# Kernel optimization log

Hardware: AMD Instinct MI355X
Metric: run time of the kernel (lower is better)

## Reference

```python
import jax, jax.numpy as jnp
import numpy as np

N, D_IN, D_OUT, E = 8192, 2048, 2048, 8


def setup_inputs() -> dict:
    key = jax.random.key(0)
    k0, k1, k2, k3, k4, k5 = jax.random.split(key, 6)
    s = 1.0 / np.sqrt(D_IN)  # torch nn.Linear default init range
    return {
        "inputs": jax.random.normal(k0, (N, D_IN), jnp.float32),
        "condition": jax.random.normal(k1, (N, D_IN), jnp.float32),
        "Wp": jax.random.uniform(k2, (E, D_IN), jnp.float32, -s, s),
        "bp": jax.random.uniform(k3, (E,), jnp.float32, -s, s),
        "We": jax.random.uniform(k4, (E, D_OUT, D_IN), jnp.float32, -s, s),
        "be": jax.random.uniform(k5, (E, D_OUT), jnp.float32, -s, s),
    }


def reference(inputs, condition, Wp, bp, We, be):
    # predictor: gating logits [N, E]
    prediction = condition @ Wp.T + bp
    # straight-through multiplier: value == 1, gradient flows to prediction
    multiply = jnp.ones_like(prediction) + (prediction - jax.lax.stop_gradient(prediction))
    # run ALL experts on the full batch (faithful to the original): [E, N, F]
    expert_out = jnp.einsum('nd,efd->enf', inputs, We) + be[:, None, :]
    combined = multiply.T[:, :, None] * expert_out  # [E, N, F]
    # select the argmax expert per row
    idx = jnp.argmax(prediction, axis=-1)  # [N]
    result = combined[idx, jnp.arange(prediction.shape[0])]  # [N, F]
    return result
```

## Files before the change

kernel.cpp:

```cpp
#include <hip/hip_runtime.h>
#include <hip/hip_bf16.h>
#include <stdint.h>

#define N_ROWS 8192
#define DIN 2048
#define DOUT 2048
#define NE 8

#define BM3 320
#define BN3 256
#define BK2 64
#define RT3 33
#define NBLK3 (8 * RT3)

#define BM 128
#define BN 128
#define BK 64
#define MAX_RT 71

typedef __bf16 bf16x8 __attribute__((ext_vector_type(8)));
typedef float f32x4 __attribute__((ext_vector_type(4)));

__device__ __forceinline__ uint32_t f2bf(float f) {
  uint32_t u = __builtin_bit_cast(uint32_t, f);
  uint32_t r = u + 0x7FFFu + ((u >> 16) & 1u);
  return r >> 16;
}

__device__ __forceinline__ void gl2lds16(const void* g, void* l) {
  __builtin_amdgcn_global_load_lds(
      (const __attribute__((address_space(1))) unsigned int*)g,
      (__attribute__((address_space(3))) unsigned int*)l, 16, 0, 0);
}

__global__ __launch_bounds__(256) void gate_kernel(
    const float* __restrict__ cond, const float* __restrict__ Wp,
    const float* __restrict__ bp, int* __restrict__ idx, int* __restrict__ counts)
{
  __shared__ int lc[NE];
  const int t = threadIdx.x;
  if (t < NE) lc[t] = 0;

  const int lane = t & 63;
  const int wid  = t >> 6;
  const int row  = blockIdx.x * 4 + wid;

  double acc[NE];
  #pragma unroll
  for (int e = 0; e < NE; ++e) acc[e] = 0.0;

  const float4* crow = (const float4*)(cond + (size_t)row * DIN);
  const float4* wp4  = (const float4*)Wp;
  #pragma unroll
  for (int i = 0; i < DIN / 256; ++i) {
    float4 c = crow[i * 64 + lane];
    #pragma unroll
    for (int e = 0; e < NE; ++e) {
      float4 w = wp4[e * (DIN / 4) + i * 64 + lane];
      acc[e] += (double)c.x * w.x + (double)c.y * w.y
              + (double)c.z * w.z + (double)c.w * w.w;
    }
  }
  #pragma unroll
  for (int e = 0; e < NE; ++e) {
    double v = acc[e];
    #pragma unroll
    for (int off = 32; off > 0; off >>= 1) v += __shfl_down(v, off, 64);
    acc[e] = v;
  }
  __syncthreads();
  if (lane == 0) {
    int best = 0; double bv = acc[0] + (double)bp[0];
    #pragma unroll
    for (int e = 1; e < NE; ++e) {
      double v = acc[e] + (double)bp[e];
      if (v > bv) { bv = v; best = e; }
    }
    idx[row] = best;
    atomicAdd(&lc[best], 1);
  }
  __syncthreads();
  if (t < NE && lc[t] > 0) atomicAdd(&counts[t], lc[t]);
}

__global__ void scan_kernel(const int* __restrict__ counts, int* __restrict__ offsets) {
  if (threadIdx.x == 0 && blockIdx.x == 0) {
    int s = 0;
    for (int e = 0; e < NE; ++e) { offsets[e] = s; s += counts[e]; }
  }
}

__global__ __launch_bounds__(256) void scatter_kernel(
    const int* __restrict__ idx, const int* __restrict__ offsets,
    int* __restrict__ fill, int* __restrict__ rows)
{
  __shared__ int lc[NE], lb[NE];
  const int t = threadIdx.x;
  if (t < NE) lc[t] = 0;
  __syncthreads();
  int n = blockIdx.x * 256 + t;
  int e = idx[n];
  int my = atomicAdd(&lc[e], 1);
  __syncthreads();
  if (t < NE) lb[t] = (lc[t] > 0) ? atomicAdd(&fill[t], lc[t]) : 0;
  __syncthreads();
  rows[offsets[e] + lb[e] + my] = n;
}

__global__ __launch_bounds__(256) void conv_kernel(
    const float* __restrict__ src, __hip_bfloat16* __restrict__ dst, size_t nchunks)
{
  const size_t stride = (size_t)gridDim.x * 256;
  for (size_t c = (size_t)blockIdx.x * 256 + threadIdx.x; c < nchunks; c += stride) {
    float4 v0 = ((const float4*)src)[c * 2];
    float4 v1 = ((const float4*)src)[c * 2 + 1];
    uint4 o;
    o.x = f2bf(v0.x) | (f2bf(v0.y) << 16);
    o.y = f2bf(v0.z) | (f2bf(v0.w) << 16);
    o.z = f2bf(v1.x) | (f2bf(v1.y) << 16);
    o.w = f2bf(v1.z) | (f2bf(v1.w) << 16);
    ((uint4*)dst)[c] = o;
  }
}

__global__ __launch_bounds__(512, 1) void moe_gemm8(
    const __hip_bfloat16* __restrict__ Xb, const __hip_bfloat16* __restrict__ Web,
    const float* __restrict__ be, const int* __restrict__ counts,
    const int* __restrict__ rows, float* __restrict__ out)
{
  __shared__ __align__(16) __hip_bfloat16 Asm[2][2][160 * 64];
  __shared__ __align__(16) __hip_bfloat16 Bsm[2][2][128 * 64];
  __shared__ int rowid[BM3];

  const int bid = blockIdx.x;
  const int w = (bid & 7) * RT3 + (bid >> 3);
  const int ct = w / RT3;
  const int rt = w % RT3;

  int e = 0, racc = 0, cnt = 0, base = 0;
  for (; e < NE; ++e) {
    cnt = counts[e];
    int tiles = (cnt + BM3 - 1) / BM3;
    if (rt < racc + tiles) break;
    racc += tiles; base += cnt;
  }
  if (e == NE) return;
  const int row0 = (rt - racc) * BM3;
  const int tid = threadIdx.x;
  if (tid < BM3)
    rowid[tid] = (row0 + tid < cnt) ? rows[base + row0 + tid] : -1;
  __syncthreads();

  const int lane = tid & 63, wid = tid >> 6;
  const bool w4 = (wid < 4);
  const int wm = wid >> 2, wn = wid & 3;
  const int g = lane >> 4, fr = lane & 15;
  const int rsw = fr * 64 + ((g ^ ((fr >> 1) & 3)) << 4);

  const int cA0 = w4 ? (3 * wid) : (12 + 2 * (wid - 4));
  const int cA1 = cA0 + 1;
  const int cA2 = cA0 + 2;
  const int cB0 = 2 * wid, cB1 = cB0 + 1;

  const int aD0 = cA0 * 1024 + lane * 16;
  const int aD1 = cA1 * 1024 + lane * 16;
  const int aD2 = cA2 * 1024 + lane * 16;
  const int bD0 = cB0 * 1024 + lane * 16;
  const int bD1 = cB1 * 1024 + lane * 16;

  const int frs = lane >> 2;
  const int qx  = (lane & 3) ^ ((lane >> 3) & 3);
  const __hip_bfloat16 *aP[2][3], *bP[2][2];
  {
    const int cA[3] = {cA0, cA1, cA2};
    const int cB[2] = {cB0, cB1};
    #pragma unroll
    for (int h = 0; h < 2; ++h) {
      #pragma unroll
      for (int s = 0; s < 3; ++s) {
        int c = cA[s];
        int R = h * 160 + (c >> 1) * 16 + frs;
        int gr = rowid[R];
        if (gr < 0) gr = 0;
        aP[h][s] = Xb + (size_t)gr * DIN + (c & 1) * 32 + qx * 8;
      }
      #pragma unroll
      for (int s = 0; s < 2; ++s) {
        int c = cB[s];
        size_t wrow = (size_t)e * DOUT + ct * BN3 + h * 128 + (c >> 1) * 16 + frs;
        bP[h][s] = Web + wrow * DIN + (c & 1) * 32 + qx * 8;
      }
    }
  }

  f32x4 acc[2][2][5][2];
  #pragma unroll
  for (int a = 0; a < 2; ++a)
    #pragma unroll
    for (int b = 0; b < 2; ++b)
      #pragma unroll
      for (int m = 0; m < 5; ++m)
        #pragma unroll
        for (int n = 0; n < 2; ++n)
          acc[a][b][m][n] = 0.0f;

  bf16x8 av[2][5], bv[2][2];

#define STG_A(buf, h, kel) do {                                              \
    gl2lds16(aP[h][0] + (kel), (char*)&Asm[buf][h][0] + aD0);                \
    gl2lds16(aP[h][1] + (kel), (char*)&Asm[buf][h][0] + aD1);                \
    if (w4) gl2lds16(aP[h][2] + (kel), (char*)&Asm[buf][h][0] + aD2);        \
  } while (0)
#define STG_B(buf, h, kel) do {                                              \
    gl2lds16(bP[h][0] + (kel), (char*)&Bsm[buf][h][0] + bD0);                \
    gl2lds16(bP[h][1] + (kel), (char*)&Bsm[buf][h][0] + bD1); } while (0)

#define READ_A(c, h) do { const char* Ab_ = (const char*)&Asm[c][h][0];      \
    _Pragma("unroll") for (int kk = 0; kk < 2; ++kk)                         \
    _Pragma("unroll") for (int mi = 0; mi < 5; ++mi)                         \
      av[kk][mi] = *(const bf16x8*)(Ab_ + (wm * 5 + mi) * 2048 + kk * 1024 + rsw); } while (0)

#define READ_B(c, h) do { const char* Bb_ = (const char*)&Bsm[c][h][0];      \
    _Pragma("unroll") for (int kk = 0; kk < 2; ++kk)                         \
    _Pragma("unroll") for (int ni = 0; ni < 2; ++ni)                         \
      bv[kk][ni] = *(const bf16x8*)(Bb_ + (wn * 2 + ni) * 2048 + kk * 1024 + rsw); } while (0)

#define BAR   __builtin_amdgcn_s_barrier()
#define LGKM0 do { asm volatile("s_waitcnt lgkmcnt(0)" ::: "memory");        \
                   __builtin_amdgcn_sched_barrier(0); } while (0)
#define VMCN  do { if (w4) { asm volatile("s_waitcnt vmcnt(5)" ::: "memory"); } \
                   else    { asm volatile("s_waitcnt vmcnt(4)" ::: "memory"); } \
                   __builtin_amdgcn_sched_barrier(0); } while (0)
#define VMC0  do { asm volatile("s_waitcnt vmcnt(0)" ::: "memory");          \
                   __builtin_amdgcn_sched_barrier(0); } while (0)

#define MFMA_PH(mh, nh) do { __builtin_amdgcn_s_setprio(1);                  \
    _Pragma("unroll") for (int kk = 0; kk < 2; ++kk)                         \
    _Pragma("unroll") for (int mi = 0; mi < 5; ++mi)                         \
    _Pragma("unroll") for (int ni = 0; ni < 2; ++ni)                         \
      acc[mh][nh][mi][ni] = __builtin_amdgcn_mfma_f32_16x16x32_bf16(         \
          av[kk][mi], bv[kk][ni], acc[mh][nh][mi][ni], 0, 0, 0);             \
    __builtin_amdgcn_s_setprio(0); } while (0)

  STG_A(0, 0, 0);  STG_B(0, 0, 0);  STG_A(0, 1, 0);  STG_B(0, 1, 0);
  STG_A(1, 0, 64); STG_B(1, 0, 64);
  VMCN;
  BAR;

  const int T = DIN / BK2;
  #pragma unroll 1
  for (int t = 0; t < T; ++t) {
    const int c = t & 1, o = c ^ 1;
    const int k1 = (t + 1) * BK2, k2 = (t + 2) * BK2;
    const bool s1 = (t + 1 < T), s2 = (t + 2 < T);

    READ_A(c, 0); READ_B(c, 0);
    if (s1) STG_A(o, 1, k1);
    BAR; LGKM0;
    MFMA_PH(0, 0);
    BAR;

    READ_B(c, 1);
    if (s1) STG_B(o, 1, k1);
    BAR; LGKM0;
    MFMA_PH(0, 1);
    BAR;

    READ_A(c, 1); READ_B(c, 0);
    if (s2) STG_A(c, 0, k2);
    BAR; LGKM0;
    MFMA_PH(1, 0);
    BAR;

    READ_B(c, 1);
    if (s2) STG_B(c, 0, k2);
    BAR; LGKM0;
    MFMA_PH(1, 1);
    if (s2) { VMCN; } else { VMC0; }
    BAR;
  }

#undef STG_A
#undef STG_B
#undef READ_A
#undef READ_B
#undef MFMA_PH

  float beh[2][2];
  #pragma unroll
  for (int nh = 0; nh < 2; ++nh)
    #pragma unroll
    for (int ni = 0; ni < 2; ++ni)
      beh[nh][ni] = be[(size_t)e * DOUT + ct * BN3 + nh * 128 + wn * 32 + ni * 16 + fr];

  #pragma unroll
  for (int mh = 0; mh < 2; ++mh)
    #pragma unroll
    for (int mi = 0; mi < 5; ++mi)
      #pragma unroll
      for (int j = 0; j < 4; ++j) {
        int R = mh * 160 + wm * 80 + mi * 16 + g * 4 + j;
        int grow = rowid[R];
        if (grow < 0) continue;
        float* orow = out + (size_t)grow * DOUT + ct * BN3;
        #pragma unroll
        for (int nh = 0; nh < 2; ++nh)
          #pragma unroll
          for (int ni = 0; ni < 2; ++ni)
            orow[nh * 128 + wn * 32 + ni * 16 + fr] = acc[mh][nh][mi][ni][j] + beh[nh][ni];
      }
}

__global__ __launch_bounds__(256) void moe_gemm_fb(
    const float* __restrict__ X, const float* __restrict__ We,
    const float* __restrict__ be, const int* __restrict__ counts,
    const int* __restrict__ offsets, const int* __restrict__ rows,
    float* __restrict__ out)
{
  __shared__ __align__(16) unsigned char Asb[BM * BK * 2];
  __shared__ __align__(16) unsigned char Bsb[BN * BK * 2];
  __shared__ int rowid[BM];

  const int ct = blockIdx.x;
  const int rt = blockIdx.y;

  int e = 0, racc = 0, cnt = 0;
  for (; e < NE; ++e) {
    cnt = counts[e];
    int tiles = (cnt + BM - 1) / BM;
    if (rt < racc + tiles) break;
    racc += tiles;
  }
  if (e == NE) return;
  const int row0 = (rt - racc) * BM;
  const int base = offsets[e];

  if (threadIdx.x < BM) {
    int r = row0 + threadIdx.x;
    rowid[threadIdx.x] = (r < cnt) ? rows[base + r] : -1;
  }
  __syncthreads();

  const int t    = threadIdx.x;
  const int lane = t & 63;
  const int wv   = t >> 6;
  const int wr   = wv >> 1, wc = wv & 1;
  const int g    = lane >> 4, fr = lane & 15;
  const int srow = t >> 4;
  const int skq  = t & 15;

  f32x4 acc[4][4];
  #pragma unroll
  for (int m = 0; m < 4; ++m)
    #pragma unroll
    for (int n = 0; n < 4; ++n)
      acc[m][n] = 0.0f;

  const size_t bcol0 = (size_t)e * DOUT + (size_t)ct * BN;

  for (int k0 = 0; k0 < DIN; k0 += BK) {
    #pragma unroll
    for (int p = 0; p < 8; ++p) {
      int r = p * 16 + srow;
      int gr = rowid[r];
      float4 v = make_float4(0.f, 0.f, 0.f, 0.f);
      if (gr >= 0)
        v = *(const float4*)(X + (size_t)gr * DIN + k0 + skq * 4);
      uint32_t w0 = f2bf(v.x) | (f2bf(v.y) << 16);
      uint32_t w1 = f2bf(v.z) | (f2bf(v.w) << 16);
      int byte = r * (BK * 2) + ((skq * 8) ^ ((r & 7) << 4));
      *(uint2*)(Asb + byte) = make_uint2(w0, w1);
    }
    #pragma unroll
    for (int p = 0; p < 8; ++p) {
      int r = p * 16 + srow;
      float4 v = *(const float4*)(We + (bcol0 + r) * DIN + k0 + skq * 4);
      uint32_t w0 = f2bf(v.x) | (f2bf(v.y) << 16);
      uint32_t w1 = f2bf(v.z) | (f2bf(v.w) << 16);
      int byte = r * (BK * 2) + ((skq * 8) ^ ((r & 7) << 4));
      *(uint2*)(Bsb + byte) = make_uint2(w0, w1);
    }
    __syncthreads();

    #pragma unroll
    for (int kk = 0; kk < BK; kk += 32) {
      bf16x8 av[4], bv[4];
      #pragma unroll
      for (int m = 0; m < 4; ++m) {
        int r = wr * 64 + m * 16 + fr;
        int byte = r * (BK * 2) + ((((kk + g * 8) * 2)) ^ ((r & 7) << 4));
        av[m] = *(const bf16x8*)(Asb + byte);
      }
      #pragma unroll
      for (int n = 0; n < 4; ++n) {
        int c = wc * 64 + n * 16 + fr;
        int byte = c * (BK * 2) + ((((kk + g * 8) * 2)) ^ ((c & 7) << 4));
        bv[n] = *(const bf16x8*)(Bsb + byte);
      }
      #pragma unroll
      for (int m = 0; m < 4; ++m)
        #pragma unroll
        for (int n = 0; n < 4; ++n)
          acc[m][n] = __builtin_amdgcn_mfma_f32_16x16x32_bf16(av[m], bv[n], acc[m][n], 0, 0, 0);
    }
    __syncthreads();
  }

  const float* berow = be + (size_t)e * DOUT + (size_t)ct * BN + wc * 64;
  #pragma unroll
  for (int m = 0; m < 4; ++m) {
    #pragma unroll
    for (int j = 0; j < 4; ++j) {
      int r = wr * 64 + m * 16 + g * 4 + j;
      int grow = rowid[r];
      if (grow < 0) continue;
      float* orow = out + (size_t)grow * DOUT + (size_t)ct * BN + wc * 64;
      #pragma unroll
      for (int n = 0; n < 4; ++n)
        orow[n * 16 + fr] = acc[m][n][j] + berow[n * 16 + fr];
    }
  }
}

extern "C" void kernel_launch(void* const* d_in, const int* in_sizes, int n_in,
                              void* d_out, int out_size, void* d_ws, size_t ws_size,
                              hipStream_t stream) {
  const float* X    = (const float*)d_in[0];
  const float* cond = (const float*)d_in[1];
  const float* Wp   = (const float*)d_in[2];
  const float* bp   = (const float*)d_in[3];
  const float* We   = (const float*)d_in[4];
  const float* be   = (const float*)d_in[5];
  float* out = (float*)d_out;

  int* counts  = (int*)d_ws;
  int* offsets = counts + 8;
  int* fill    = counts + 16;
  int* idx     = (int*)((char*)d_ws + 256);
  int* rows    = idx + N_ROWS;
  const size_t XB_OFF  = 65792;
  const size_t WEB_OFF = XB_OFF + (size_t)N_ROWS * DIN * 2;
  const size_t WS_NEED = WEB_OFF + (size_t)NE * DOUT * DIN * 2;

  hipMemsetAsync(d_ws, 0, 256, stream);
  gate_kernel<<<N_ROWS / 4, 256, 0, stream>>>(cond, Wp, bp, idx, counts);
  scan_kernel<<<1, 64, 0, stream>>>(counts, offsets);
  scatter_kernel<<<N_ROWS / 256, 256, 0, stream>>>(idx, offsets, fill, rows);

  if (ws_size >= WS_NEED) {
    __hip_bfloat16* Xb  = (__hip_bfloat16*)((char*)d_ws + XB_OFF);
    __hip_bfloat16* Web = (__hip_bfloat16*)((char*)d_ws + WEB_OFF);
    conv_kernel<<<2048, 256, 0, stream>>>(X, Xb, (size_t)N_ROWS * DIN / 8);
    conv_kernel<<<2048, 256, 0, stream>>>(We, Web, (size_t)NE * DOUT * DIN / 8);
    moe_gemm8<<<NBLK3, 512, 0, stream>>>(Xb, Web, be, counts, rows, out);
  } else {
    moe_gemm_fb<<<dim3(DOUT / BN, MAX_RT), 256, 0, stream>>>(X, We, be, counts, offsets, rows, out);
  }
}
```

Before: 197.2 us.

## Fuse expert weight bf16 conversion into GEMM B-tile staging

Drops the separate pass that converted the full fp32 expert weight tensor to bf16. The GEMM now loads fp32 weight tiles into registers, converts them, and writes them to LDS, with restructured vmcnt waits to keep the prefetch pipeline. This removes a full read-write pass over the weights and shrinks workspace, at the cost of more global bytes per B tile, register-staged loads instead of direct-to-LDS, and extra conversion ALU work inside the main loop.

```diff
diff --git a/kernel.cpp b/kernel.cpp
--- a/kernel.cpp
+++ b/kernel.cpp
@@ -124,7 +124,7 @@
 }
 
 __global__ __launch_bounds__(512, 1) void moe_gemm8(
-    const __hip_bfloat16* __restrict__ Xb, const __hip_bfloat16* __restrict__ Web,
+    const __hip_bfloat16* __restrict__ Xb, const float* __restrict__ We,
     const float* __restrict__ be, const int* __restrict__ counts,
     const int* __restrict__ rows, float* __restrict__ out)
 {
@@ -170,7 +170,8 @@
 
   const int frs = lane >> 2;
   const int qx  = (lane & 3) ^ ((lane >> 3) & 3);
-  const __hip_bfloat16 *aP[2][3], *bP[2][2];
+  const __hip_bfloat16 *aP[2][3];
+  const float *bPf[2][2];
   {
     const int cA[3] = {cA0, cA1, cA2};
     const int cB[2] = {cB0, cB1};
@@ -188,7 +189,7 @@
       for (int s = 0; s < 2; ++s) {
         int c = cB[s];
         size_t wrow = (size_t)e * DOUT + ct * BN3 + h * 128 + (c >> 1) * 16 + frs;
-        bP[h][s] = Web + wrow * DIN + (c & 1) * 32 + qx * 8;
+        bPf[h][s] = We + wrow * DIN + (c & 1) * 32 + qx * 8;
       }
     }
   }
@@ -205,15 +206,32 @@
           acc[a][b][m][n] = 0.0f;
 
   bf16x8 av[2][5], bv[2][2];
+  float4 br1[4], br2[4];
 
 #define STG_A(buf, h, kel) do {                                              \
     gl2lds16(aP[h][0] + (kel), (char*)&Asm[buf][h][0] + aD0);                \
     gl2lds16(aP[h][1] + (kel), (char*)&Asm[buf][h][0] + aD1);                \
     if (w4) gl2lds16(aP[h][2] + (kel), (char*)&Asm[buf][h][0] + aD2);        \
   } while (0)
-#define STG_B(buf, h, kel) do {                                              \
-    gl2lds16(bP[h][0] + (kel), (char*)&Bsm[buf][h][0] + bD0);                \
-    gl2lds16(bP[h][1] + (kel), (char*)&Bsm[buf][h][0] + bD1); } while (0)
+
+#define BL(dst, h, kel) do {                                                 \
+    dst[0] = *(const float4*)(bPf[h][0] + (kel));                            \
+    dst[1] = *(const float4*)(bPf[h][0] + (kel) + 4);                        \
+    dst[2] = *(const float4*)(bPf[h][1] + (kel));                            \
+    dst[3] = *(const float4*)(bPf[h][1] + (kel) + 4); } while (0)
+
+#define BW(src, buf, h) do {                                                 \
+    uint4 o0, o1;                                                            \
+    o0.x = f2bf(src[0].x) | (f2bf(src[0].y) << 16);                          \
+    o0.y = f2bf(src[0].z) | (f2bf(src[0].w) << 16);                          \
+    o0.z = f2bf(src[1].x) | (f2bf(src[1].y) << 16);                          \
+    o0.w = f2bf(src[1].z) | (f2bf(src[1].w) << 16);                          \
+    o1.x = f2bf(src[2].x) | (f2bf(src[2].y) << 16);                          \
+    o1.y = f2bf(src[2].z) | (f2bf(src[2].w) << 16);                          \
+    o1.z = f2bf(src[3].x) | (f2bf(src[3].y) << 16);                          \
+    o1.w = f2bf(src[3].z) | (f2bf(src[3].w) << 16);                          \
+    *(uint4*)((char*)&Bsm[buf][h][0] + bD0) = o0;                            \
+    *(uint4*)((char*)&Bsm[buf][h][0] + bD1) = o1; } while (0)
 
 #define READ_A(c, h) do { const char* Ab_ = (const char*)&Asm[c][h][0];      \
     _Pragma("unroll") for (int kk = 0; kk < 2; ++kk)                         \
@@ -226,13 +244,19 @@
       bv[kk][ni] = *(const bf16x8*)(Bb_ + (wn * 2 + ni) * 2048 + kk * 1024 + rsw); } while (0)
 
 #define BAR   __builtin_amdgcn_s_barrier()
-#define LGKM0 do { asm volatile("s_waitcnt lgkmcnt(0)" ::: "memory");        \
-                   __builtin_amdgcn_sched_barrier(0); } while (0)
-#define VMCN  do { if (w4) { asm volatile("s_waitcnt vmcnt(5)" ::: "memory"); } \
-                   else    { asm volatile("s_waitcnt vmcnt(4)" ::: "memory"); } \
-                   __builtin_amdgcn_sched_barrier(0); } while (0)
-#define VMC0  do { asm volatile("s_waitcnt vmcnt(0)" ::: "memory");          \
-                   __builtin_amdgcn_sched_barrier(0); } while (0)
+#define SB0   __builtin_amdgcn_sched_barrier(0)
+#define LGKM0 do { asm volatile("s_waitcnt lgkmcnt(0)" ::: "memory"); SB0; } while (0)
+#define VMC0  do { asm volatile("s_waitcnt vmcnt(0)" ::: "memory"); SB0; } while (0)
+#define VMW1_S do { if (w4) { asm volatile("s_waitcnt vmcnt(7)" ::: "memory"); }  \
+                    else    { asm volatile("s_waitcnt vmcnt(6)" ::: "memory"); }  \
+                    SB0; } while (0)
+#define VMW1_L do { asm volatile("s_waitcnt vmcnt(2)" ::: "memory"); SB0; } while (0)
+#define VMW2   do { if (w4) { asm volatile("s_waitcnt vmcnt(6)" ::: "memory"); }  \
+                    else    { asm volatile("s_waitcnt vmcnt(4)" ::: "memory"); }  \
+                    SB0; } while (0)
+#define VMCN   do { if (w4) { asm volatile("s_waitcnt vmcnt(3)" ::: "memory"); }  \
+                    else    { asm volatile("s_waitcnt vmcnt(2)" ::: "memory"); }  \
+                    SB0; } while (0)
 
 #define MFMA_PH(mh, nh) do { __builtin_amdgcn_s_setprio(1);                  \
     _Pragma("unroll") for (int kk = 0; kk < 2; ++kk)                         \
@@ -242,9 +266,12 @@
           av[kk][mi], bv[kk][ni], acc[mh][nh][mi][ni], 0, 0, 0);             \
     __builtin_amdgcn_s_setprio(0); } while (0)
 
-  STG_A(0, 0, 0);  STG_B(0, 0, 0);  STG_A(0, 1, 0);  STG_B(0, 1, 0);
-  STG_A(1, 0, 64); STG_B(1, 0, 64);
+  BL(br1, 0, 0);  VMC0; BW(br1, 0, 0);
+  BL(br1, 1, 0);  VMC0; BW(br1, 0, 1);
+  BL(br1, 0, 64); VMC0; BW(br1, 1, 0);
+  STG_A(0, 0, 0); STG_A(0, 1, 0); STG_A(1, 0, 64);
   VMCN;
+  asm volatile("s_waitcnt lgkmcnt(0)" ::: "memory");
   BAR;
 
   const int T = DIN / BK2;
@@ -255,13 +282,17 @@
     const bool s1 = (t + 1 < T), s2 = (t + 2 < T);
 
     READ_A(c, 0); READ_B(c, 0);
+    if (s1) BL(br1, 1, k1);
+    SB0;
+    if (s2) BL(br2, 0, k2);
+    SB0;
     if (s1) STG_A(o, 1, k1);
     BAR; LGKM0;
     MFMA_PH(0, 0);
     BAR;
 
     READ_B(c, 1);
-    if (s1) STG_B(o, 1, k1);
+    if (s1) { if (s2) { VMW1_S; } else { VMW1_L; } BW(br1, o, 1); }
     BAR; LGKM0;
     MFMA_PH(0, 1);
     BAR;
@@ -273,7 +304,7 @@
     BAR;
 
     READ_B(c, 1);
-    if (s2) STG_B(c, 0, k2);
+    if (s2) { VMW2; BW(br2, c, 0); }
     BAR; LGKM0;
     MFMA_PH(1, 1);
     if (s2) { VMCN; } else { VMC0; }
@@ -281,7 +312,8 @@
   }
 
 #undef STG_A
-#undef STG_B
+#undef BL
+#undef BW
 #undef READ_A
 #undef READ_B
 #undef MFMA_PH
@@ -439,8 +471,7 @@
   int* idx     = (int*)((char*)d_ws + 256);
   int* rows    = idx + N_ROWS;
   const size_t XB_OFF  = 65792;
-  const size_t WEB_OFF = XB_OFF + (size_t)N_ROWS * DIN * 2;
-  const size_t WS_NEED = WEB_OFF + (size_t)NE * DOUT * DIN * 2;
+  const size_t WS_NEED = XB_OFF + (size_t)N_ROWS * DIN * 2;
 
   hipMemsetAsync(d_ws, 0, 256, stream);
   gate_kernel<<<N_ROWS / 4, 256, 0, stream>>>(cond, Wp, bp, idx, counts);
@@ -448,11 +479,9 @@
   scatter_kernel<<<N_ROWS / 256, 256, 0, stream>>>(idx, offsets, fill, rows);
 
   if (ws_size >= WS_NEED) {
-    __hip_bfloat16* Xb  = (__hip_bfloat16*)((char*)d_ws + XB_OFF);
-    __hip_bfloat16* Web = (__hip_bfloat16*)((char*)d_ws + WEB_OFF);
+    __hip_bfloat16* Xb = (__hip_bfloat16*)((char*)d_ws + XB_OFF);
     conv_kernel<<<2048, 256, 0, stream>>>(X, Xb, (size_t)N_ROWS * DIN / 8);
-    conv_kernel<<<2048, 256, 0, stream>>>(We, Web, (size_t)NE * DOUT * DIN / 8);
-    moe_gemm8<<<NBLK3, 512, 0, stream>>>(Xb, Web, be, counts, rows, out);
+    moe_gemm8<<<NBLK3, 512, 0, stream>>>(Xb, We, be, counts, rows, out);
   } else {
     moe_gemm_fb<<<dim3(DOUT / BN, MAX_RT), 256, 0, stream>>>(X, We, be, counts, offsets, rows, out);
   }
```

Measured after the change: 506.8 us. 2.57x slower.

## Make grouped GEMM persistent with a CU-sized grid looping over live tiles

Applied to the files above, without the earlier changes.

Launches a fixed grid of 256 blocks that loop over the actual number of row/column tiles computed from expert counts, instead of a fixed 264-block grid with early exits. Tile ordering changes so column tiles are the fastest index, grouping blocks that share the same gathered input rows. This aims to avoid a partial second wave and idle blocks, at the cost of extra barriers and per-tile setup inside the loop and different L2 reuse of weights.

```diff
diff --git a/kernel.cpp b/kernel.cpp
--- a/kernel.cpp
+++ b/kernel.cpp
@@ -10,8 +10,7 @@
 #define BM3 320
 #define BN3 256
 #define BK2 64
-#define RT3 33
-#define NBLK3 (8 * RT3)
+#define GRID3 256
 
 #define BM 128
 #define BN 128
@@ -132,25 +131,7 @@
   __shared__ __align__(16) __hip_bfloat16 Bsm[2][2][128 * 64];
   __shared__ int rowid[BM3];
 
-  const int bid = blockIdx.x;
-  const int w = (bid & 7) * RT3 + (bid >> 3);
-  const int ct = w / RT3;
-  const int rt = w % RT3;
-
-  int e = 0, racc = 0, cnt = 0, base = 0;
-  for (; e < NE; ++e) {
-    cnt = counts[e];
-    int tiles = (cnt + BM3 - 1) / BM3;
-    if (rt < racc + tiles) break;
-    racc += tiles; base += cnt;
-  }
-  if (e == NE) return;
-  const int row0 = (rt - racc) * BM3;
   const int tid = threadIdx.x;
-  if (tid < BM3)
-    rowid[tid] = (row0 + tid < cnt) ? rows[base + row0 + tid] : -1;
-  __syncthreads();
-
   const int lane = tid & 63, wid = tid >> 6;
   const bool w4 = (wid < 4);
   const int wm = wid >> 2, wn = wid & 3;
@@ -161,50 +142,26 @@
   const int cA1 = cA0 + 1;
   const int cA2 = cA0 + 2;
   const int cB0 = 2 * wid, cB1 = cB0 + 1;
-
   const int aD0 = cA0 * 1024 + lane * 16;
   const int aD1 = cA1 * 1024 + lane * 16;
   const int aD2 = cA2 * 1024 + lane * 16;
   const int bD0 = cB0 * 1024 + lane * 16;
   const int bD1 = cB1 * 1024 + lane * 16;
-
   const int frs = lane >> 2;
   const int qx  = (lane & 3) ^ ((lane >> 3) & 3);
-  const __hip_bfloat16 *aP[2][3], *bP[2][2];
-  {
-    const int cA[3] = {cA0, cA1, cA2};
-    const int cB[2] = {cB0, cB1};
-    #pragma unroll
-    for (int h = 0; h < 2; ++h) {
-      #pragma unroll
-      for (int s = 0; s < 3; ++s) {
-        int c = cA[s];
-        int R = h * 160 + (c >> 1) * 16 + frs;
-        int gr = rowid[R];
-        if (gr < 0) gr = 0;
-        aP[h][s] = Xb + (size_t)gr * DIN + (c & 1) * 32 + qx * 8;
-      }
-      #pragma unroll
-      for (int s = 0; s < 2; ++s) {
-        int c = cB[s];
-        size_t wrow = (size_t)e * DOUT + ct * BN3 + h * 128 + (c >> 1) * 16 + frs;
-        bP[h][s] = Web + wrow * DIN + (c & 1) * 32 + qx * 8;
-      }
-    }
-  }
-
-  f32x4 acc[2][2][5][2];
-  #pragma unroll
-  for (int a = 0; a < 2; ++a)
-    #pragma unroll
-    for (int b = 0; b < 2; ++b)
-      #pragma unroll
-      for (int m = 0; m < 5; ++m)
-        #pragma unroll
-        for (int n = 0; n < 2; ++n)
-          acc[a][b][m][n] = 0.0f;
-
-  bf16x8 av[2][5], bv[2][2];
+
+  int RT = 0;
+  #pragma unroll
+  for (int e = 0; e < NE; ++e) RT += (counts[e] + BM3 - 1) / BM3;
+  const int total = RT * 8;
+
+#define BAR   __builtin_amdgcn_s_barrier()
+#define SB0   __builtin_amdgcn_sched_barrier(0)
+#define LGKM0 do { asm volatile("s_waitcnt lgkmcnt(0)" ::: "memory"); SB0; } while (0)
+#define VMCN  do { if (w4) { asm volatile("s_waitcnt vmcnt(5)" ::: "memory"); } \
+                   else    { asm volatile("s_waitcnt vmcnt(4)" ::: "memory"); } \
+                   SB0; } while (0)
+#define VMC0  do { asm volatile("s_waitcnt vmcnt(0)" ::: "memory"); SB0; } while (0)
 
 #define STG_A(buf, h, kel) do {                                              \
     gl2lds16(aP[h][0] + (kel), (char*)&Asm[buf][h][0] + aD0);                \
@@ -225,15 +182,6 @@
     _Pragma("unroll") for (int ni = 0; ni < 2; ++ni)                         \
       bv[kk][ni] = *(const bf16x8*)(Bb_ + (wn * 2 + ni) * 2048 + kk * 1024 + rsw); } while (0)
 
-#define BAR   __builtin_amdgcn_s_barrier()
-#define LGKM0 do { asm volatile("s_waitcnt lgkmcnt(0)" ::: "memory");        \
-                   __builtin_amdgcn_sched_barrier(0); } while (0)
-#define VMCN  do { if (w4) { asm volatile("s_waitcnt vmcnt(5)" ::: "memory"); } \
-                   else    { asm volatile("s_waitcnt vmcnt(4)" ::: "memory"); } \
-                   __builtin_amdgcn_sched_barrier(0); } while (0)
-#define VMC0  do { asm volatile("s_waitcnt vmcnt(0)" ::: "memory");          \
-                   __builtin_amdgcn_sched_barrier(0); } while (0)
-
 #define MFMA_PH(mh, nh) do { __builtin_amdgcn_s_setprio(1);                  \
     _Pragma("unroll") for (int kk = 0; kk < 2; ++kk)                         \
     _Pragma("unroll") for (int mi = 0; mi < 5; ++mi)                         \
@@ -242,42 +190,122 @@
           av[kk][mi], bv[kk][ni], acc[mh][nh][mi][ni], 0, 0, 0);             \
     __builtin_amdgcn_s_setprio(0); } while (0)
 
-  STG_A(0, 0, 0);  STG_B(0, 0, 0);  STG_A(0, 1, 0);  STG_B(0, 1, 0);
-  STG_A(1, 0, 64); STG_B(1, 0, 64);
-  VMCN;
-  BAR;
-
-  const int T = DIN / BK2;
   #pragma unroll 1
-  for (int t = 0; t < T; ++t) {
-    const int c = t & 1, o = c ^ 1;
-    const int k1 = (t + 1) * BK2, k2 = (t + 2) * BK2;
-    const bool s1 = (t + 1 < T), s2 = (t + 2 < T);
-
-    READ_A(c, 0); READ_B(c, 0);
-    if (s1) STG_A(o, 1, k1);
-    BAR; LGKM0;
-    MFMA_PH(0, 0);
+  for (int idx = blockIdx.x; idx < total; idx += GRID3) {
+    const int ct = idx & 7;
+    const int rt = idx >> 3;
+
+    int e = 0, racc = 0, cnt = 0, base = 0;
+    for (; e < NE; ++e) {
+      cnt = counts[e];
+      int tiles = (cnt + BM3 - 1) / BM3;
+      if (rt < racc + tiles) break;
+      racc += tiles; base += cnt;
+    }
+    const int row0 = (rt - racc) * BM3;
+
+    __syncthreads();
+    if (tid < BM3)
+      rowid[tid] = (row0 + tid < cnt) ? rows[base + row0 + tid] : -1;
+    __syncthreads();
+
+    const __hip_bfloat16 *aP[2][3], *bP[2][2];
+    {
+      const int cA[3] = {cA0, cA1, cA2};
+      const int cB[2] = {cB0, cB1};
+      #pragma unroll
+      for (int h = 0; h < 2; ++h) {
+        #pragma unroll
+        for (int s = 0; s < 3; ++s) {
+          int c = cA[s];
+          int R = h * 160 + (c >> 1) * 16 + frs;
+          int gr = rowid[R];
+          if (gr < 0) gr = 0;
+          aP[h][s] = Xb + (size_t)gr * DIN + (c & 1) * 32 + qx * 8;
+        }
+        #pragma unroll
+        for (int s = 0; s < 2; ++s) {
+          int c = cB[s];
+          size_t wrow = (size_t)e * DOUT + ct * BN3 + h * 128 + (c >> 1) * 16 + frs;
+          bP[h][s] = Web + wrow * DIN + (c & 1) * 32 + qx * 8;
+        }
+      }
+    }
+
+    f32x4 acc[2][2][5][2];
+    #pragma unroll
+    for (int a = 0; a < 2; ++a)
+      #pragma unroll
+      for (int b = 0; b < 2; ++b)
+        #pragma unroll
+        for (int m = 0; m < 5; ++m)
+          #pragma unroll
+          for (int n = 0; n < 2; ++n)
+            acc[a][b][m][n] = 0.0f;
+
+    bf16x8 av[2][5], bv[2][2];
+
+    STG_A(0, 0, 0);  STG_B(0, 0, 0);  STG_A(0, 1, 0);  STG_B(0, 1, 0);
+    STG_A(1, 0, 64); STG_B(1, 0, 64);
+    VMCN;
     BAR;
 
-    READ_B(c, 1);
-    if (s1) STG_B(o, 1, k1);
-    BAR; LGKM0;
-    MFMA_PH(0, 1);
-    BAR;
-
-    READ_A(c, 1); READ_B(c, 0);
-    if (s2) STG_A(c, 0, k2);
-    BAR; LGKM0;
-    MFMA_PH(1, 0);
-    BAR;
-
-    READ_B(c, 1);
-    if (s2) STG_B(c, 0, k2);
-    BAR; LGKM0;
-    MFMA_PH(1, 1);
-    if (s2) { VMCN; } else { VMC0; }
-    BAR;
+    const int T = DIN / BK2;
+    #pragma unroll 1
+    for (int t = 0; t < T; ++t) {
+      const int c = t & 1, o = c ^ 1;
+      const int k1 = (t + 1) * BK2, k2 = (t + 2) * BK2;
+      const bool s1 = (t + 1 < T), s2 = (t + 2 < T);
+
+      READ_A(c, 0); READ_B(c, 0);
+      if (s1) STG_A(o, 1, k1);
+      BAR; LGKM0;
+      MFMA_PH(0, 0);
+      BAR;
+
+      READ_B(c, 1);
+      if (s1) STG_B(o, 1, k1);
+      BAR; LGKM0;
+      MFMA_PH(0, 1);
+      BAR;
+
+      READ_A(c, 1); READ_B(c, 0);
+      if (s2) STG_A(c, 0, k2);
+      BAR; LGKM0;
+      MFMA_PH(1, 0);
+      BAR;
+
+      READ_B(c, 1);
+      if (s2) STG_B(c, 0, k2);
+      BAR; LGKM0;
+      MFMA_PH(1, 1);
+      if (s2) { VMCN; } else { VMC0; }
+      BAR;
+    }
+
+    float beh[2][2];
+    #pragma unroll
+    for (int nh = 0; nh < 2; ++nh)
+      #pragma unroll
+      for (int ni = 0; ni < 2; ++ni)
+        beh[nh][ni] = be[(size_t)e * DOUT + ct * BN3 + nh * 128 + wn * 32 + ni * 16 + fr];
+
+    #pragma unroll
+    for (int mh = 0; mh < 2; ++mh)
+      #pragma unroll
+      for (int mi = 0; mi < 5; ++mi)
+        #pragma unroll
+        for (int j = 0; j < 4; ++j) {
+          int R = mh * 160 + wm * 80 + mi * 16 + g * 4 + j;
+          int grow = rowid[R];
+          if (grow < 0) continue;
+          float* orow = out + (size_t)grow * DOUT + ct * BN3;
+          #pragma unroll
+          for (int nh = 0; nh < 2; ++nh)
+            #pragma unroll
+            for (int ni = 0; ni < 2; ++ni)
+              orow[nh * 128 + wn * 32 + ni * 16 + fr] = acc[mh][nh][mi][ni][j] + beh[nh][ni];
+        }
   }
 
 #undef STG_A
@@ -285,30 +313,11 @@
 #undef READ_A
 #undef READ_B
 #undef MFMA_PH
-
-  float beh[2][2];
-  #pragma unroll
-  for (int nh = 0; nh < 2; ++nh)
-    #pragma unroll
-    for (int ni = 0; ni < 2; ++ni)
-      beh[nh][ni] = be[(size_t)e * DOUT + ct * BN3 + nh * 128 + wn * 32 + ni * 16 + fr];
-
-  #pragma unroll
-  for (int mh = 0; mh < 2; ++mh)
-    #pragma unroll
-    for (int mi = 0; mi < 5; ++mi)
-      #pragma unroll
-      for (int j = 0; j < 4; ++j) {
-        int R = mh * 160 + wm * 80 + mi * 16 + g * 4 + j;
-        int grow = rowid[R];
-        if (grow < 0) continue;
-        float* orow = out + (size_t)grow * DOUT + ct * BN3;
-        #pragma unroll
-        for (int nh = 0; nh < 2; ++nh)
-          #pragma unroll
-          for (int ni = 0; ni < 2; ++ni)
-            orow[nh * 128 + wn * 32 + ni * 16 + fr] = acc[mh][nh][mi][ni][j] + beh[nh][ni];
-      }
+#undef BAR
+#undef SB0
+#undef LGKM0
+#undef VMCN
+#undef VMC0
 }
 
 __global__ __launch_bounds__(256) void moe_gemm_fb(
@@ -452,7 +461,7 @@
     __hip_bfloat16* Web = (__hip_bfloat16*)((char*)d_ws + WEB_OFF);
     conv_kernel<<<2048, 256, 0, stream>>>(X, Xb, (size_t)N_ROWS * DIN / 8);
     conv_kernel<<<2048, 256, 0, stream>>>(We, Web, (size_t)NE * DOUT * DIN / 8);
-    moe_gemm8<<<NBLK3, 512, 0, stream>>>(Xb, Web, be, counts, rows, out);
+    moe_gemm8<<<GRID3, 512, 0, stream>>>(Xb, Web, be, counts, rows, out);
   } else {
     moe_gemm_fb<<<dim3(DOUT / BN, MAX_RT), 256, 0, stream>>>(X, We, be, counts, offsets, rows, out);
   }
```

Measured after the change: 208.2 us. 1.06x slower.
